# Optimization experiments

Measured on AMD Instinct MI355X. Metric: run time of the kernel, lower is better.

## Reference

```python
import jax, jax.numpy as jnp
import numpy as np

B, L, M, IS = 64, 20, 16, 1024  # batch, headers/example, tokens/header, feature dim
EPS = 1e-12


def setup_inputs() -> dict:
    key = jax.random.key(0)
    ks = jax.random.split(key, 10)
    total = B * L
    s = 1.0 / np.sqrt(IS)
    return {
        "ctx": jax.random.normal(ks[0], (B, IS), jnp.float32),
        "wemb_hpu": jax.random.normal(ks[1], (total, M, IS), jnp.float32),
        "l_hpu": jnp.full((total,), M, jnp.int32),
        "l_hs": jnp.full((B,), L, jnp.int32),
        "U_w": jax.random.uniform(ks[2], (IS, IS), jnp.float32, -s, s),
        "U_b": jnp.zeros((IS,), jnp.float32),
        "V_w": jax.random.uniform(ks[3], (IS, IS), jnp.float32, -s, s),
        "V_b": jnp.zeros((IS,), jnp.float32),
        "enc_w": jax.random.uniform(ks[4], (IS, 2 * IS), jnp.float32, -s, s),
        "enc_b": jnp.zeros((IS,), jnp.float32),
        "gamma": jnp.ones((IS,), jnp.float32),
        "beta": jnp.zeros((IS,), jnp.float32),
    }


def reference(ctx, wemb_hpu, l_hpu, l_hs, U_w, U_b, V_w, V_b, enc_w, enc_b, gamma, beta):
    total = wemb_hpu.shape[0]
    bS = ctx.shape[0]
    seg = jnp.repeat(jnp.arange(bS), total // bS)  # header-unit -> example id (constant l_hs)
    wenc_u = ctx @ U_w.T + U_b                      # [B, IS]
    wenc_v = wemb_hpu @ V_w.T + V_b                 # [T, M, IS]
    # per-header attention over its M tokens: sum over feature dim, softmax over tokens
    attn = jnp.einsum('ti,tmi->tm', wenc_u[seg], wenc_v)   # [T, M]
    p = jax.nn.softmax(attn, axis=1)
    pooled = jnp.einsum('tm,tmi->ti', p, wemb_hpu)          # [T, IS]
    cat = jnp.concatenate([pooled, ctx[seg]], axis=-1)      # [T, 2*IS]
    h = cat @ enc_w.T + enc_b                               # [T, IS]
    # scatter into padded [B, mL_hs, IS] (constant lengths -> exact reshape)
    wenc_hs = h.reshape(bS, total // bS, -1)
    # TF-style LayerNorm (eps inside sqrt)
    u = wenc_hs.mean(-1, keepdims=True)
    s2 = ((wenc_hs - u) ** 2).mean(-1, keepdims=True)
    x = (wenc_hs - u) / jnp.sqrt(s2 + EPS)
    return gamma * x + beta
```

## Files before the change

kernel.cpp:

```cpp
#include <hip/hip_runtime.h>
#include <math.h>

#define TPB 256

constexpr int ISZ = 1024;
constexpr int NB  = 64;
constexpr int NL  = 20;
constexpr int NM  = 16;
constexpr int NT  = NB * NL;

typedef __attribute__((ext_vector_type(8))) short  bf16x8;
typedef __attribute__((ext_vector_type(4))) float  f32x4;

struct Args {
    const float *ctx, *wemb, *U_w, *U_b, *V_w, *enc_w, *enc_b, *gamma, *beta;
    float *Upart, *Cpart, *uvpart, *cenc, *out;
    unsigned short *Vth, *Vtl, *encb, *pooledb;
};

__device__ __forceinline__ unsigned short f2bf(float x) {
    unsigned int u = __builtin_bit_cast(unsigned int, x);
    unsigned int r = (u + 0x7fff + ((u >> 16) & 1)) >> 16;
    return (unsigned short)r;
}
__device__ __forceinline__ float bf2f(unsigned short h) {
    unsigned int u = ((unsigned int)h) << 16;
    return __builtin_bit_cast(float, u);
}
__device__ __forceinline__ void split4(float4 v, ushort4& h, ushort4& l) {
    h.x = f2bf(v.x); l.x = f2bf(v.x - bf2f(h.x));
    h.y = f2bf(v.y); l.y = f2bf(v.y - bf2f(h.y));
    h.z = f2bf(v.z); l.z = f2bf(v.z - bf2f(h.z));
    h.w = f2bf(v.w); l.w = f2bf(v.w - bf2f(h.w));
}
__device__ __forceinline__ void gld_lds16(const void* g, void* l) {
    __builtin_amdgcn_global_load_lds(
        (const __attribute__((address_space(1))) unsigned int*)g,
        (__attribute__((address_space(3))) unsigned int*)l, 16, 0, 0);
}

__device__ __forceinline__ void stage_hl(const float* __restrict__ src, int ld,
                                         int kbeg, unsigned char* ldsH,
                                         unsigned char* ldsL, int tid)
{
    #pragma unroll
    for (int r = 0; r < 4; ++r) {
        int idx = r * 256 + tid;
        int row = idx >> 4, cg4 = (idx & 15) << 2;
        float4 v = *(const float4*)&src[(size_t)row * ld + kbeg + cg4];
        ushort4 h, l; split4(v, h, l);
        int boff = row * 128 + ((cg4 << 1) ^ ((row & 7) << 4));
        *(ushort4*)(ldsH + boff) = h;
        *(ushort4*)(ldsL + boff) = l;
    }
}
__device__ __forceinline__ void stage_h(const float* __restrict__ src, int ld,
                                        int kbeg, unsigned char* ldsH, int tid)
{
    #pragma unroll
    for (int r = 0; r < 4; ++r) {
        int idx = r * 256 + tid;
        int row = idx >> 4, cg4 = (idx & 15) << 2;
        float4 v = *(const float4*)&src[(size_t)row * ld + kbeg + cg4];
        ushort4 h = { f2bf(v.x), f2bf(v.y), f2bf(v.z), f2bf(v.w) };
        int boff = row * 128 + ((cg4 << 1) ^ ((row & 7) << 4));
        *(ushort4*)(ldsH + boff) = h;
    }
}
__device__ __forceinline__ void stage_A_uv(const float* __restrict__ Upart,
                                           const float* __restrict__ U_b,
                                           int kbeg, unsigned char* ldsH,
                                           unsigned char* ldsL, int tid)
{
    #pragma unroll
    for (int r = 0; r < 4; ++r) {
        int idx = r * 256 + tid;
        int row = idx >> 4, cg4 = (idx & 15) << 2;
        int k = kbeg + cg4;
        float4 v = *(const float4*)&U_b[k];
        #pragma unroll
        for (int s = 0; s < 8; ++s) {
            float4 u = *(const float4*)&Upart[(size_t)(s * 64 + row) * ISZ + k];
            v.x += u.x; v.y += u.y; v.z += u.z; v.w += u.w;
        }
        ushort4 h, l; split4(v, h, l);
        int boff = row * 128 + ((cg4 << 1) ^ ((row & 7) << 4));
        *(ushort4*)(ldsH + boff) = h;
        *(ushort4*)(ldsL + boff) = l;
    }
}

__device__ __forceinline__ void comp_hl(const unsigned char* lds, f32x4 acc[2][2], int tid)
{
    const int wid = tid >> 6, lane = tid & 63;
    const int ln = lane & 15, kb = lane >> 4;
    const int wr = wid >> 1, wc = wid & 1;
    #pragma unroll
    for (int ks = 0; ks < 2; ++ks) {
        const int cb = ks * 64 + kb * 16;
        bf16x8 ah[2], al[2], bh[2], bl[2];
        #pragma unroll
        for (int m = 0; m < 2; ++m) {
            int ra = wr * 32 + m * 16 + ln;
            int off = ra * 128 + (cb ^ ((ra & 7) << 4));
            ah[m] = *(const bf16x8*)(lds + off);
            al[m] = *(const bf16x8*)(lds + 8192 + off);
        }
        #pragma unroll
        for (int n = 0; n < 2; ++n) {
            int rb = wc * 32 + n * 16 + ln;
            int off = rb * 128 + (cb ^ ((rb & 7) << 4));
            bh[n] = *(const bf16x8*)(lds + 16384 + off);
            bl[n] = *(const bf16x8*)(lds + 24576 + off);
        }
        #pragma unroll
        for (int m = 0; m < 2; ++m)
            #pragma unroll
            for (int n = 0; n < 2; ++n) {
                acc[m][n] = __builtin_amdgcn_mfma_f32_16x16x32_bf16(ah[m], bh[n], acc[m][n], 0, 0, 0);
                acc[m][n] = __builtin_amdgcn_mfma_f32_16x16x32_bf16(ah[m], bl[n], acc[m][n], 0, 0, 0);
                acc[m][n] = __builtin_amdgcn_mfma_f32_16x16x32_bf16(al[m], bh[n], acc[m][n], 0, 0, 0);
            }
    }
}
__device__ __forceinline__ void comp_h(const unsigned char* lds, f32x4 acc[2][2], int tid)
{
    const int wid = tid >> 6, lane = tid & 63;
    const int ln = lane & 15, kb = lane >> 4;
    const int wr = wid >> 1, wc = wid & 1;
    #pragma unroll
    for (int ks = 0; ks < 2; ++ks) {
        const int cb = ks * 64 + kb * 16;
        bf16x8 ah[2], bh[2];
        #pragma unroll
        for (int m = 0; m < 2; ++m) {
            int ra = wr * 32 + m * 16 + ln;
            ah[m] = *(const bf16x8*)(lds + ra * 128 + (cb ^ ((ra & 7) << 4)));
        }
        #pragma unroll
        for (int n = 0; n < 2; ++n) {
            int rb = wc * 32 + n * 16 + ln;
            bh[n] = *(const bf16x8*)(lds + 16384 + rb * 128 + (cb ^ ((rb & 7) << 4)));
        }
        #pragma unroll
        for (int m = 0; m < 2; ++m)
            #pragma unroll
            for (int n = 0; n < 2; ++n)
                acc[m][n] = __builtin_amdgcn_mfma_f32_16x16x32_bf16(ah[m], bh[n], acc[m][n], 0, 0, 0);
    }
}

__global__ __launch_bounds__(TPB)
void k_prep(Args A)
{
    __shared__ __align__(16) unsigned char smem[32768];
    const int bid = blockIdx.x, tid = threadIdx.x;
    const int wid = tid >> 6, lane = tid & 63;
    const int wr = wid >> 1, wc = wid & 1;
    const int cl = lane & 15, rg = lane >> 4;

    if (bid < 256) {
        const bool isU = (bid < 128);
        const int id = isU ? bid : bid - 128;
        const int s = id >> 4, n0 = (id & 15) * 64;
        const int kbeg = s * 128;
        f32x4 acc[2][2] = {};
        for (int kt = 0; kt < 2; ++kt) {
            const int kk = kbeg + kt * 64;
            if (isU) {
                stage_hl(A.ctx, ISZ, kk, smem, smem + 8192, tid);
                stage_hl(A.U_w + (size_t)n0 * ISZ, ISZ, kk, smem + 16384, smem + 24576, tid);
            } else {
                stage_h(A.ctx, ISZ, kk, smem, tid);
                stage_h(A.enc_w + (size_t)n0 * 2048 + 1024, 2048, kk, smem + 16384, tid);
            }
            __syncthreads();
            if (isU) comp_hl(smem, acc, tid);
            else     comp_h(smem, acc, tid);
            __syncthreads();
        }
        float* dst = isU ? A.Upart : A.Cpart;
        #pragma unroll
        for (int m = 0; m < 2; ++m)
            #pragma unroll
            for (int n = 0; n < 2; ++n) {
                int col = n0 + wc * 32 + n * 16 + cl;
                #pragma unroll
                for (int j = 0; j < 4; ++j) {
                    int row = wr * 32 + m * 16 + rg * 4 + j;
                    dst[(size_t)(s * 64 + row) * ISZ + col] = acc[m][n][j];
                }
            }
    } else if (bid < 512) {
        float (*t)[65] = (float(*)[65])smem;
        const int id = bid - 256;
        const int r0 = (id >> 4) * 64, c0 = (id & 15) * 64;
        const int tr = tid >> 4, tc = (tid & 15) * 4;
        #pragma unroll
        for (int i = 0; i < 4; ++i) {
            float4 v = *(const float4*)&A.V_w[(size_t)(r0 + tr + 16 * i) * ISZ + c0 + tc];
            t[tr + 16 * i][tc + 0] = v.x; t[tr + 16 * i][tc + 1] = v.y;
            t[tr + 16 * i][tc + 2] = v.z; t[tr + 16 * i][tc + 3] = v.w;
        }
        __syncthreads();
        #pragma unroll
        for (int i = 0; i < 4; ++i) {
            int rr = tr + 16 * i;
            float4 v = { t[tc + 0][rr], t[tc + 1][rr], t[tc + 2][rr], t[tc + 3][rr] };
            ushort4 h, l; split4(v, h, l);
            *(ushort4*)&A.Vth[(size_t)(c0 + rr) * ISZ + r0 + tc] = h;
            *(ushort4*)&A.Vtl[(size_t)(c0 + rr) * ISZ + r0 + tc] = l;
        }
    } else {
        const int id = bid - 512;
        const int c = tid << 2;
        #pragma unroll
        for (int r = 0; r < 8; ++r) {
            int row = id * 8 + r;
            float4 v = *(const float4*)&A.enc_w[(size_t)row * 2048 + c];
            ushort4 o = { f2bf(v.x), f2bf(v.y), f2bf(v.z), f2bf(v.w) };
            *(ushort4*)&A.encb[(size_t)row * ISZ + c] = o;
        }
    }
}

__global__ __launch_bounds__(TPB)
void k_mid(Args A)
{
    __shared__ __align__(16) unsigned char smem[32768];
    const int bid = blockIdx.x, tid = threadIdx.x;
    const int wid = tid >> 6, lane = tid & 63;

    if (bid < 128) {
        const int s = bid >> 4, n0 = (bid & 15) * 64;
        const int kbeg = s * 128;
        const int srow = lane >> 3, sbyte = (lane & 7) << 4;
        const int swz = sbyte ^ (srow << 4);
        f32x4 acc[2][2] = {};
        for (int kt = 0; kt < 2; ++kt) {
            const int kk = kbeg + kt * 64;
            const int kbyte = kk * 2;
            #pragma unroll
            for (int i = 0; i < 2; ++i) {
                int r = wid * 8 + i * 32 + srow;
                size_t gb = (size_t)(n0 + r) * 2048 + kbyte + swz;
                gld_lds16((const char*)A.Vth + gb, (void*)(smem + 16384 + wid * 1024 + i * 4096));
                gld_lds16((const char*)A.Vtl + gb, (void*)(smem + 24576 + wid * 1024 + i * 4096));
            }
            stage_A_uv(A.Upart, A.U_b, kk, smem, smem + 8192, tid);
            __syncthreads();
            comp_hl(smem, acc, tid);
            __syncthreads();
        }
        const int wr = wid >> 1, wc = wid & 1;
        const int cl = lane & 15, rg = lane >> 4;
        #pragma unroll
        for (int m = 0; m < 2; ++m)
            #pragma unroll
            for (int n = 0; n < 2; ++n) {
                int col = n0 + wc * 32 + n * 16 + cl;
                #pragma unroll
                for (int j = 0; j < 4; ++j) {
                    int row = wr * 32 + m * 16 + rg * 4 + j;
                    A.uvpart[(size_t)(s * 64 + row) * ISZ + col] = acc[m][n][j];
                }
            }
    } else {
        const int row0 = (bid - 128) * 4;
        const int c = tid << 2;
        #pragma unroll
        for (int r = 0; r < 4; ++r) {
            int row = row0 + r;
            float4 v = *(const float4*)&A.enc_b[c];
            #pragma unroll
            for (int s = 0; s < 8; ++s) {
                float4 u = *(const float4*)&A.Cpart[(size_t)(s * 64 + row) * ISZ + c];
                v.x += u.x; v.y += u.y; v.z += u.z; v.w += u.w;
            }
            *(float4*)&A.cenc[(size_t)row * ISZ + c] = v;
        }
    }
}

__global__ __launch_bounds__(TPB)
void k_attn(Args A)
{
    __shared__ float red[16][4];
    __shared__ float att[16];
    const int t = blockIdx.x;
    const int b = t / NL;
    const int tid = threadIdx.x;
    const int lane = tid & 63, wid = tid >> 6;

    const float* w = A.wemb + (size_t)t * NM * ISZ;
    const int j0 = tid << 2;

    float4 u4 = {0.f, 0.f, 0.f, 0.f};
    #pragma unroll
    for (int s = 0; s < 8; ++s) {
        float4 u = *(const float4*)&A.uvpart[(size_t)(s * 64 + b) * ISZ + j0];
        u4.x += u.x; u4.y += u.y; u4.z += u.z; u4.w += u.w;
    }

    float4 wv[NM];
    float part[NM];
    #pragma unroll
    for (int m = 0; m < NM; ++m) {
        wv[m] = *(const float4*)&w[m * ISZ + j0];
        part[m] = wv[m].x * u4.x + wv[m].y * u4.y + wv[m].z * u4.z + wv[m].w * u4.w;
    }
    #pragma unroll
    for (int m = 0; m < NM; ++m) {
        float v = part[m];
        #pragma unroll
        for (int off = 32; off > 0; off >>= 1) v += __shfl_down(v, off, 64);
        if (lane == 0) red[m][wid] = v;
    }
    __syncthreads();
    if (tid < NM) att[tid] = red[tid][0] + red[tid][1] + red[tid][2] + red[tid][3];
    __syncthreads();

    float mx = att[0];
    #pragma unroll
    for (int m = 1; m < NM; ++m) mx = fmaxf(mx, att[m]);
    float p[NM], sm = 0.0f;
    #pragma unroll
    for (int m = 0; m < NM; ++m) { p[m] = __expf(att[m] - mx); sm += p[m]; }
    float inv = 1.0f / sm;

    float4 acc = {0.0f, 0.0f, 0.0f, 0.0f};
    #pragma unroll
    for (int m = 0; m < NM; ++m) {
        float pm = p[m] * inv;
        acc.x += pm * wv[m].x; acc.y += pm * wv[m].y;
        acc.z += pm * wv[m].z; acc.w += pm * wv[m].w;
    }
    ushort4 o;
    o.x = f2bf(acc.x); o.y = f2bf(acc.y); o.z = f2bf(acc.z); o.w = f2bf(acc.w);
    *(ushort4*)&A.pooledb[(size_t)t * ISZ + j0] = o;
}

__global__ __launch_bounds__(TPB)
void k_enc(Args A)
{
    __shared__ __align__(16) unsigned char smem[24576];
    const int tid  = threadIdx.x;
    const int wid  = tid >> 6, lane = tid & 63;
    const int m0   = (blockIdx.x >> 4) * 128;
    const int n0   = (blockIdx.x & 15) * 64;
    const int ln   = lane & 15, kb = lane >> 4;
    const int wr   = wid >> 1, wc = wid & 1;
    const int srow = lane >> 3, sbyte = (lane & 7) << 4;
    const int swz  = sbyte ^ (srow << 4);

    f32x4 acc[4][2] = {};
    const char* Abase = (const char*)A.pooledb;
    const char* Bbase = (const char*)A.encb;

    for (int kt = 0; kt < 16; ++kt) {
        const int kbyte = kt * 128;
        #pragma unroll
        for (int i = 0; i < 4; ++i) {
            int r = wid * 8 + i * 32 + srow;
            gld_lds16(Abase + ((size_t)(m0 + r) * ISZ) * 2 + kbyte + swz,
                      (void*)(smem + wid * 1024 + i * 4096));
        }
        #pragma unroll
        for (int i = 0; i < 2; ++i) {
            int r = wid * 8 + i * 32 + srow;
            gld_lds16(Bbase + ((size_t)(n0 + r) * ISZ) * 2 + kbyte + swz,
                      (void*)(smem + 16384 + wid * 1024 + i * 4096));
        }
        __syncthreads();
        #pragma unroll
        for (int ks = 0; ks < 2; ++ks) {
            const int cb = (ks * 64 + kb * 16);
            bf16x8 a[4], b[2];
            #pragma unroll
            for (int m = 0; m < 4; ++m) {
                int ra = wr * 64 + m * 16 + ln;
                a[m] = *(const bf16x8*)(smem + ra * 128 + (cb ^ ((ra & 7) << 4)));
            }
            #pragma unroll
            for (int n = 0; n < 2; ++n) {
                int rb = wc * 32 + n * 16 + ln;
                b[n] = *(const bf16x8*)(smem + 16384 + rb * 128 + (cb ^ ((rb & 7) << 4)));
            }
            #pragma unroll
            for (int m = 0; m < 4; ++m)
                #pragma unroll
                for (int n = 0; n < 2; ++n)
                    acc[m][n] = __builtin_amdgcn_mfma_f32_16x16x32_bf16(a[m], b[n], acc[m][n], 0, 0, 0);
        }
        __syncthreads();
    }

    const int cl = lane & 15, rg = lane >> 4;
    #pragma unroll
    for (int m = 0; m < 4; ++m) {
        #pragma unroll
        for (int n = 0; n < 2; ++n) {
            int col = n0 + wc * 32 + n * 16 + cl;
            #pragma unroll
            for (int j = 0; j < 4; ++j) {
                int row = m0 + wr * 64 + m * 16 + rg * 4 + j;
                A.out[(size_t)row * ISZ + col] = acc[m][n][j] + A.cenc[(size_t)(row / NL) * ISZ + col];
            }
        }
    }
}

__global__ __launch_bounds__(TPB)
void k_ln(Args A)
{
    __shared__ float rs[4], rs2[4];
    __shared__ float mu_s, rstd_s;
    const int t = blockIdx.x;
    const int tid = threadIdx.x;
    const int lane = tid & 63, wid = tid >> 6;
    const int c = tid << 2;

    float4 v = *(const float4*)&A.out[(size_t)t * ISZ + c];
    float s  = v.x + v.y + v.z + v.w;
    float s2 = v.x * v.x + v.y * v.y + v.z * v.z + v.w * v.w;
    #pragma unroll
    for (int off = 32; off > 0; off >>= 1) {
        s  += __shfl_down(s, off, 64);
        s2 += __shfl_down(s2, off, 64);
    }
    if (lane == 0) { rs[wid] = s; rs2[wid] = s2; }
    __syncthreads();
    if (tid == 0) {
        float S  = rs[0] + rs[1] + rs[2] + rs[3];
        float S2 = rs2[0] + rs2[1] + rs2[2] + rs2[3];
        float m  = S / ISZ;
        float var = S2 / ISZ - m * m;
        mu_s  = m;
        rstd_s = rsqrtf(var + 1e-12f);
    }
    __syncthreads();
    const float mu = mu_s, rstd = rstd_s;
    float4 g  = *(const float4*)&A.gamma[c];
    float4 be = *(const float4*)&A.beta[c];
    float4 o;
    o.x = g.x * (v.x - mu) * rstd + be.x;
    o.y = g.y * (v.y - mu) * rstd + be.y;
    o.z = g.z * (v.z - mu) * rstd + be.z;
    o.w = g.w * (v.w - mu) * rstd + be.w;
    *(float4*)&A.out[(size_t)t * ISZ + c] = o;
}

extern "C" void kernel_launch(void* const* d_in, const int* in_sizes, int n_in,
                              void* d_out, int out_size, void* d_ws, size_t ws_size,
                              hipStream_t stream)
{
    Args A;
    A.ctx   = (const float*)d_in[0];
    A.wemb  = (const float*)d_in[1];
    A.U_w   = (const float*)d_in[4];
    A.U_b   = (const float*)d_in[5];
    A.V_w   = (const float*)d_in[6];
    A.enc_w = (const float*)d_in[8];
    A.enc_b = (const float*)d_in[9];
    A.gamma = (const float*)d_in[10];
    A.beta  = (const float*)d_in[11];
    A.out   = (float*)d_out;

    float* ws = (float*)d_ws;
    A.Upart  = ws;
    A.Cpart  = A.Upart  + 8 * NB * ISZ;
    A.uvpart = A.Cpart  + 8 * NB * ISZ;
    A.cenc   = A.uvpart + 8 * NB * ISZ;
    unsigned short* p = (unsigned short*)(A.cenc + NB * ISZ);
    A.Vth     = p;  p += ISZ * ISZ;
    A.Vtl     = p;  p += ISZ * ISZ;
    A.encb    = p;  p += ISZ * ISZ;
    A.pooledb = p;

    k_prep<<<640, TPB, 0, stream>>>(A);
    k_mid <<<144, TPB, 0, stream>>>(A);
    k_attn<<<NT,  TPB, 0, stream>>>(A);
    k_enc <<<160, TPB, 0, stream>>>(A);
    k_ln  <<<NT,  TPB, 0, stream>>>(A);
}
```

Before: 61.21 us.

## Replace split-K partial buffers with atomics and full-K ctx-encoder blocks

The ctx@enc_w second-half GEMM moves from 128 split-K blocks plus a reduction pass to 16 full-K blocks that add the bias and write cenc directly. The uv GEMM now accumulates its 8 K-slices into a zeroed buffer with atomicAdd, so the attention kernel reads one row instead of summing 8 partials. Extra blocks in the prep kernel zero the uv buffer. This removes partial-buffer traffic and the reduction work, but the ctx-encoder GEMM runs on only 16 long-running blocks, atomics make the float sums order-nondeterministic, and the uv zeroing depends on kernel order.

```diff
diff --git a/kernel.cpp b/kernel.cpp
--- a/kernel.cpp
+++ b/kernel.cpp
@@ -14,7 +14,7 @@
 
 struct Args {
     const float *ctx, *wemb, *U_w, *U_b, *V_w, *enc_w, *enc_b, *gamma, *beta;
-    float *Upart, *Cpart, *uvpart, *cenc, *out;
+    float *uv, *Upart, *cenc, *out;
     unsigned short *Vth, *Vtl, *encb, *pooledb;
 };
 
@@ -159,27 +159,18 @@
     const int wr = wid >> 1, wc = wid & 1;
     const int cl = lane & 15, rg = lane >> 4;
 
-    if (bid < 256) {
-        const bool isU = (bid < 128);
-        const int id = isU ? bid : bid - 128;
-        const int s = id >> 4, n0 = (id & 15) * 64;
+    if (bid < 128) {
+        const int s = bid >> 4, n0 = (bid & 15) * 64;
         const int kbeg = s * 128;
         f32x4 acc[2][2] = {};
         for (int kt = 0; kt < 2; ++kt) {
             const int kk = kbeg + kt * 64;
-            if (isU) {
-                stage_hl(A.ctx, ISZ, kk, smem, smem + 8192, tid);
-                stage_hl(A.U_w + (size_t)n0 * ISZ, ISZ, kk, smem + 16384, smem + 24576, tid);
-            } else {
-                stage_h(A.ctx, ISZ, kk, smem, tid);
-                stage_h(A.enc_w + (size_t)n0 * 2048 + 1024, 2048, kk, smem + 16384, tid);
-            }
+            stage_hl(A.ctx, ISZ, kk, smem, smem + 8192, tid);
+            stage_hl(A.U_w + (size_t)n0 * ISZ, ISZ, kk, smem + 16384, smem + 24576, tid);
             __syncthreads();
-            if (isU) comp_hl(smem, acc, tid);
-            else     comp_h(smem, acc, tid);
+            comp_hl(smem, acc, tid);
             __syncthreads();
         }
-        float* dst = isU ? A.Upart : A.Cpart;
         #pragma unroll
         for (int m = 0; m < 2; ++m)
             #pragma unroll
@@ -188,12 +179,34 @@
                 #pragma unroll
                 for (int j = 0; j < 4; ++j) {
                     int row = wr * 32 + m * 16 + rg * 4 + j;
-                    dst[(size_t)(s * 64 + row) * ISZ + col] = acc[m][n][j];
+                    A.Upart[(size_t)(s * 64 + row) * ISZ + col] = acc[m][n][j];
                 }
             }
-    } else if (bid < 512) {
+    } else if (bid < 144) {
+        const int n0 = (bid - 128) * 64;
+        f32x4 acc[2][2] = {};
+        for (int kt = 0; kt < 16; ++kt) {
+            const int kk = kt * 64;
+            stage_h(A.ctx, ISZ, kk, smem, tid);
+            stage_h(A.enc_w + (size_t)n0 * 2048 + 1024, 2048, kk, smem + 16384, tid);
+            __syncthreads();
+            comp_h(smem, acc, tid);
+            __syncthreads();
+        }
+        #pragma unroll
+        for (int m = 0; m < 2; ++m)
+            #pragma unroll
+            for (int n = 0; n < 2; ++n) {
+                int col = n0 + wc * 32 + n * 16 + cl;
+                #pragma unroll
+                for (int j = 0; j < 4; ++j) {
+                    int row = wr * 32 + m * 16 + rg * 4 + j;
+                    A.cenc[(size_t)row * ISZ + col] = acc[m][n][j] + A.enc_b[col];
+                }
+            }
+    } else if (bid < 400) {
         float (*t)[65] = (float(*)[65])smem;
-        const int id = bid - 256;
+        const int id = bid - 144;
         const int r0 = (id >> 4) * 64, c0 = (id & 15) * 64;
         const int tr = tid >> 4, tc = (tid & 15) * 4;
         #pragma unroll
@@ -211,8 +224,8 @@
             *(ushort4*)&A.Vth[(size_t)(c0 + rr) * ISZ + r0 + tc] = h;
             *(ushort4*)&A.Vtl[(size_t)(c0 + rr) * ISZ + r0 + tc] = l;
         }
-    } else {
-        const int id = bid - 512;
+    } else if (bid < 528) {
+        const int id = bid - 400;
         const int c = tid << 2;
         #pragma unroll
         for (int r = 0; r < 8; ++r) {
@@ -221,65 +234,58 @@
             ushort4 o = { f2bf(v.x), f2bf(v.y), f2bf(v.z), f2bf(v.w) };
             *(ushort4*)&A.encb[(size_t)row * ISZ + c] = o;
         }
+    } else {
+        const int id = bid - 528;
+        float4 z = {0.f, 0.f, 0.f, 0.f};
+        #pragma unroll
+        for (int r = 0; r < 4; ++r) {
+            int i4 = ((id * TPB + tid) * 4 + r) * 4;
+            *(float4*)&A.uv[i4] = z;
+        }
     }
 }
 
 __global__ __launch_bounds__(TPB)
-void k_mid(Args A)
+void k_uv(Args A)
 {
     __shared__ __align__(16) unsigned char smem[32768];
-    const int bid = blockIdx.x, tid = threadIdx.x;
+    const int tid = threadIdx.x;
+    const int bid = blockIdx.x;
     const int wid = tid >> 6, lane = tid & 63;
-
-    if (bid < 128) {
-        const int s = bid >> 4, n0 = (bid & 15) * 64;
-        const int kbeg = s * 128;
-        const int srow = lane >> 3, sbyte = (lane & 7) << 4;
-        const int swz = sbyte ^ (srow << 4);
-        f32x4 acc[2][2] = {};
-        for (int kt = 0; kt < 2; ++kt) {
-            const int kk = kbeg + kt * 64;
-            const int kbyte = kk * 2;
-            #pragma unroll
-            for (int i = 0; i < 2; ++i) {
-                int r = wid * 8 + i * 32 + srow;
-                size_t gb = (size_t)(n0 + r) * 2048 + kbyte + swz;
-                gld_lds16((const char*)A.Vth + gb, (void*)(smem + 16384 + wid * 1024 + i * 4096));
-                gld_lds16((const char*)A.Vtl + gb, (void*)(smem + 24576 + wid * 1024 + i * 4096));
-            }
-            stage_A_uv(A.Upart, A.U_b, kk, smem, smem + 8192, tid);
-            __syncthreads();
-            comp_hl(smem, acc, tid);
-            __syncthreads();
-        }
-        const int wr = wid >> 1, wc = wid & 1;
-        const int cl = lane & 15, rg = lane >> 4;
-        #pragma unroll
-        for (int m = 0; m < 2; ++m)
-            #pragma unroll
-            for (int n = 0; n < 2; ++n) {
-                int col = n0 + wc * 32 + n * 16 + cl;
-                #pragma unroll
-                for (int j = 0; j < 4; ++j) {
-                    int row = wr * 32 + m * 16 + rg * 4 + j;
-                    A.uvpart[(size_t)(s * 64 + row) * ISZ + col] = acc[m][n][j];
-                }
-            }
-    } else {
-        const int row0 = (bid - 128) * 4;
-        const int c = tid << 2;
-        #pragma unroll
-        for (int r = 0; r < 4; ++r) {
-            int row = row0 + r;
-            float4 v = *(const float4*)&A.enc_b[c];
-            #pragma unroll
-            for (int s = 0; s < 8; ++s) {
-                float4 u = *(const float4*)&A.Cpart[(size_t)(s * 64 + row) * ISZ + c];
-                v.x += u.x; v.y += u.y; v.z += u.z; v.w += u.w;
-            }
-            *(float4*)&A.cenc[(size_t)row * ISZ + c] = v;
-        }
-    }
+    const int s = bid >> 4, n0 = (bid & 15) * 64;
+    const int kbeg = s * 128;
+    const int srow = lane >> 3, sbyte = (lane & 7) << 4;
+    const int swz = sbyte ^ (srow << 4);
+
+    f32x4 acc[2][2] = {};
+    for (int kt = 0; kt < 2; ++kt) {
+        const int kk = kbeg + kt * 64;
+        const int kbyte = kk * 2;
+        #pragma unroll
+        for (int i = 0; i < 2; ++i) {
+            int r = wid * 8 + i * 32 + srow;
+            size_t gb = (size_t)(n0 + r) * 2048 + kbyte + swz;
+            gld_lds16((const char*)A.Vth + gb, (void*)(smem + 16384 + wid * 1024 + i * 4096));
+            gld_lds16((const char*)A.Vtl + gb, (void*)(smem + 24576 + wid * 1024 + i * 4096));
+        }
+        stage_A_uv(A.Upart, A.U_b, kk, smem, smem + 8192, tid);
+        __syncthreads();
+        comp_hl(smem, acc, tid);
+        __syncthreads();
+    }
+    const int wr = wid >> 1, wc = wid & 1;
+    const int cl = lane & 15, rg = lane >> 4;
+    #pragma unroll
+    for (int m = 0; m < 2; ++m)
+        #pragma unroll
+        for (int n = 0; n < 2; ++n) {
+            int col = n0 + wc * 32 + n * 16 + cl;
+            #pragma unroll
+            for (int j = 0; j < 4; ++j) {
+                int row = wr * 32 + m * 16 + rg * 4 + j;
+                atomicAdd(&A.uv[(size_t)row * ISZ + col], acc[m][n][j]);
+            }
+        }
 }
 
 __global__ __launch_bounds__(TPB)
@@ -294,13 +300,7 @@
 
     const float* w = A.wemb + (size_t)t * NM * ISZ;
     const int j0 = tid << 2;
-
-    float4 u4 = {0.f, 0.f, 0.f, 0.f};
-    #pragma unroll
-    for (int s = 0; s < 8; ++s) {
-        float4 u = *(const float4*)&A.uvpart[(size_t)(s * 64 + b) * ISZ + j0];
-        u4.x += u.x; u4.y += u.y; u4.z += u.z; u4.w += u.w;
-    }
+    float4 u4 = *(const float4*)&A.uv[(size_t)b * ISZ + j0];
 
     float4 wv[NM];
     float part[NM];
@@ -467,18 +467,17 @@
     A.out   = (float*)d_out;
 
     float* ws = (float*)d_ws;
-    A.Upart  = ws;
-    A.Cpart  = A.Upart  + 8 * NB * ISZ;
-    A.uvpart = A.Cpart  + 8 * NB * ISZ;
-    A.cenc   = A.uvpart + 8 * NB * ISZ;
+    A.uv    = ws;
+    A.Upart = ws + NB * ISZ;
+    A.cenc  = A.Upart + 8 * NB * ISZ;
     unsigned short* p = (unsigned short*)(A.cenc + NB * ISZ);
     A.Vth     = p;  p += ISZ * ISZ;
     A.Vtl     = p;  p += ISZ * ISZ;
     A.encb    = p;  p += ISZ * ISZ;
     A.pooledb = p;
 
-    k_prep<<<640, TPB, 0, stream>>>(A);
-    k_mid <<<144, TPB, 0, stream>>>(A);
+    k_prep<<<544, TPB, 0, stream>>>(A);
+    k_uv  <<<128, TPB, 0, stream>>>(A);
     k_attn<<<NT,  TPB, 0, stream>>>(A);
     k_enc <<<160, TPB, 0, stream>>>(A);
     k_ln  <<<NT,  TPB, 0, stream>>>(A);
```

New measurement: 73.12 us. 19.5% more time.
